# Optimization experiments

Measured on AMD Instinct MI355X. Metric: run time of the kernel, lower is better.

The kernel has to match this reference:

```python
import jax, jax.numpy as jnp
import numpy as np

N_NODES = 100000
N_EDGES = 3200000
F_IN, F_HID, F_OUT = 25, 16, 2


def gcn_conv(x, edge_index, W, b, n_nodes):
    """PyG GCNConv: out = D^-1/2 (A + I) D^-1/2 (x W) + b."""
    h = x @ W  # [N, F_out] transform first (small feature dim)
    loops = jnp.arange(n_nodes, dtype=edge_index.dtype)
    row = jnp.concatenate([edge_index[0], loops])  # sources j
    col = jnp.concatenate([edge_index[1], loops])  # targets i
    ones = jnp.ones(row.shape[0], dtype=h.dtype)
    deg = jax.ops.segment_sum(ones, col, num_segments=n_nodes)
    dinv = jnp.where(deg > 0, jax.lax.rsqrt(jnp.maximum(deg, 1.0)), 0.0)
    norm = dinv[row] * dinv[col]  # [E+N]
    msgs = h[row] * norm[:, None]  # gather + scale
    out = jax.ops.segment_sum(msgs, col, num_segments=n_nodes)
    return out + b


def setup_inputs() -> dict:
    key = jax.random.key(0)
    k1, k2, k3, k4, k5, k6 = jax.random.split(key, 6)
    x = jax.random.normal(k1, (N_NODES, F_IN), dtype=jnp.float32)
    edge_index = jax.random.randint(k2, (2, N_EDGES), 0, N_NODES, dtype=jnp.int64)
    s1 = 1.0 / np.sqrt(F_IN)
    s2 = 1.0 / np.sqrt(F_HID)
    W1 = jax.random.uniform(k3, (F_IN, F_HID), jnp.float32, -s1, s1)
    b1 = jax.random.uniform(k4, (F_HID,), jnp.float32, -s1, s1)
    W2 = jax.random.uniform(k5, (F_HID, F_OUT), jnp.float32, -s2, s2)
    b2 = jax.random.uniform(k6, (F_OUT,), jnp.float32, -s2, s2)
    return {"x": x, "edge_index": edge_index, "W1": W1, "b1": b1, "W2": W2, "b2": b2}


def reference(x, edge_index, W1, b1, W2, b2):
    n = x.shape[0]
    h = jax.nn.relu(gcn_conv(x, edge_index, W1, b1, n))
    h = gcn_conv(h, edge_index, W2, b2, n)
    return jax.nn.log_softmax(h, axis=1)
```

## Files before the change

kernel.cpp:

```cpp
#include <hip/hip_runtime.h>
#include <hip/hip_fp16.h>
#include <math.h>

#define THREADS 256
#define NPB 1024
#define SHIFT 10
#define MASK 1023
#define MAX_BINS 128
#define CAPE 36864
#define BIN_BLOCKS 512


__global__ void __launch_bounds__(256) k_bin(const int* __restrict__ row,
                                             const int* __restrict__ col,
                                             int e, int* __restrict__ binCnt,
                                             int* __restrict__ binned) {
    __shared__ int hist[MAX_BINS];
    __shared__ int cur[MAX_BINS];
    __shared__ int baseg[MAX_BINS];
    __shared__ int lofs[MAX_BINS];
    __shared__ int scn[MAX_BINS];
    extern __shared__ int dyn[];
    int per = (((e + (int)gridDim.x - 1) / (int)gridDim.x) + 3) & ~3;
    int e0 = blockIdx.x * per;
    if (e0 >= e) return;
    int e1 = min(e0 + per, e);
    int cntL = e1 - e0;
    int* sbuf  = dyn;
    int* sbuf2 = dyn + per;
    unsigned char* sbin = (unsigned char*)(dyn + 2 * per);
    int tid = threadIdx.x;
    for (int t = tid; t < MAX_BINS; t += 256) { hist[t] = 0; cur[t] = 0; }
    __syncthreads();
    int nq = cntL >> 2;
    const int4* r4 = (const int4*)(row + e0);
    const int4* c4 = (const int4*)(col + e0);
    for (int q = tid; q < nq; q += 256) {
        int4 r = r4[q], c = c4[q];
        int b0 = c.x >> SHIFT, b1 = c.y >> SHIFT, b2 = c.z >> SHIFT, b3 = c.w >> SHIFT;
        ((int4*)sbuf)[q] = make_int4((r.x << SHIFT) | (c.x & MASK),
                                     (r.y << SHIFT) | (c.y & MASK),
                                     (r.z << SHIFT) | (c.z & MASK),
                                     (r.w << SHIFT) | (c.w & MASK));
        *((uchar4*)(sbin + q * 4)) = make_uchar4((unsigned char)b0, (unsigned char)b1,
                                                 (unsigned char)b2, (unsigned char)b3);
        atomicAdd(&hist[b0], 1); atomicAdd(&hist[b1], 1);
        atomicAdd(&hist[b2], 1); atomicAdd(&hist[b3], 1);
    }
    for (int li = (nq << 2) + tid; li < cntL; li += 256) {
        int c = col[e0 + li], r = row[e0 + li], b = c >> SHIFT;
        sbuf[li] = (r << SHIFT) | (c & MASK);
        sbin[li] = (unsigned char)b;
        atomicAdd(&hist[b], 1);
    }
    __syncthreads();
    if (tid < MAX_BINS) {
        int h = hist[tid];
        baseg[tid] = (h > 0) ? atomicAdd(&binCnt[tid], h) : 0;
        scn[tid] = h;
    }
    __syncthreads();
    for (int off = 1; off < MAX_BINS; off <<= 1) {
        int a = (tid >= off && tid < MAX_BINS) ? scn[tid - off] : 0;
        __syncthreads();
        if (tid < MAX_BINS) scn[tid] += a;
        __syncthreads();
    }
    if (tid < MAX_BINS) lofs[tid] = scn[tid] - hist[tid];
    __syncthreads();
    for (int li = tid; li < cntL; li += 256) {
        int b = sbin[li];
        int p = lofs[b] + atomicAdd(&cur[b], 1);
        sbuf2[p] = sbuf[li];
    }
    __syncthreads();
    int wv = tid >> 6, ln = tid & 63;
    for (int b = wv; b < MAX_BINS; b += 4) {
        int len = hist[b];
        int lo = lofs[b];
        int gb = baseg[b];
        for (int i = ln; i < len; i += 64) {
            int pos = gb + i;
            if (pos < CAPE) binned[b * CAPE + pos] = sbuf2[lo + i];
        }
    }
}


__global__ void __launch_bounds__(1024) k_sort(const int* __restrict__ binned,
                                               const int* __restrict__ binCnt,
                                               int* __restrict__ csr,
                                               int* __restrict__ gptr,
                                               int* __restrict__ gcnt,
                                               float* __restrict__ dinv, int n) {
    __shared__ int cnt[NPB];
    __shared__ int scn[NPB];
    int b = blockIdx.x;
    int t = threadIdx.x;
    cnt[t] = 0;
    __syncthreads();
    int m = min(binCnt[b], CAPE);
    const int* eb = binned + b * CAPE;
    for (int i = t; i < m; i += 1024)
        atomicAdd(&cnt[eb[i] & MASK], 1);
    __syncthreads();
    int v = cnt[t];
    scn[t] = v;
    __syncthreads();
    for (int off = 1; off < NPB; off <<= 1) {
        int a = (t >= off) ? scn[t - off] : 0;
        __syncthreads();
        scn[t] += a;
        __syncthreads();
    }
    int excl = scn[t] - v;
    int node = b * NPB + t;
    if (node < n) {
        gptr[node] = b * CAPE + excl;
        gcnt[node] = v;
        dinv[node] = rsqrtf((float)(v + 1));
    }
    cnt[t] = excl;
    __syncthreads();
    for (int i = t; i < m; i += 1024) {
        int e = eb[i];
        int slot = atomicAdd(&cnt[e & MASK], 1);
        csr[b * CAPE + slot] = e >> SHIFT;
    }
}

__global__ void __launch_bounds__(256) k_xform1(const float* __restrict__ x,
                                                const float* __restrict__ W1,
                                                const float* __restrict__ dinv,
                                                __half* __restrict__ z1h, int n) {
    __shared__ float sW[25 * 16];
    __shared__ float tile[4][64 * 25];
    int w = threadIdx.x >> 6, lane = threadIdx.x & 63;
    for (int t = threadIdx.x; t < 25 * 16; t += 256) sW[t] = W1[t];
    long blockRow = (long)blockIdx.x * 256;
    long waveRow = blockRow + w * 64;
    const float* src = x + waveRow * 25;
    long rem = (long)n * 25 - waveRow * 25;
#pragma unroll
    for (int k = 0; k < 25; k++) {
        int idx = k * 64 + lane;
        tile[w][idx] = (idx < rem) ? src[idx] : 0.f;
    }
    __syncthreads();
    long node = blockRow + threadIdx.x;
    if (node >= n) return;
    float xi[25];
#pragma unroll
    for (int k = 0; k < 25; k++) xi[k] = tile[w][lane * 25 + k];
    float di = dinv[node];
    union { int4 v[2]; __half h[16]; } u;
#pragma unroll
    for (int c = 0; c < 16; c++) {
        float a = 0.f;
#pragma unroll
        for (int k = 0; k < 25; k++) a = fmaf(xi[k], sW[k * 16 + c], a);
        u.h[c] = __float2half(a * di);
    }
    int4* o = (int4*)(z1h + node * 16);
    o[0] = u.v[0];
    o[1] = u.v[1];
}

__global__ void k_gather1(const int* __restrict__ ptr, const int* __restrict__ cnt,
                          const int* __restrict__ csr, const __half* __restrict__ z1h,
                          const float* __restrict__ dinv,
                          const float* __restrict__ b1, const float* __restrict__ W2,
                          __half2* __restrict__ z2h, int n) {
    int g = threadIdx.x >> 3;
    int c2 = threadIdx.x & 7;
    int node = blockIdx.x * 32 + g;
    if (node >= n) return;
    const __half2* z1p = (const __half2*)z1h;
    int beg = ptr[node], d = cnt[node];
    __half2 sv = z1p[(size_t)node * 8 + c2];
    float a0 = __low2float(sv), a1 = __high2float(sv);
    int e = 0;
    for (; e + 4 <= d; e += 4) {
        int s0 = csr[beg + e], s1 = csr[beg + e + 1];
        int s2 = csr[beg + e + 2], s3 = csr[beg + e + 3];
        __half2 v0 = z1p[(size_t)s0 * 8 + c2];
        __half2 v1 = z1p[(size_t)s1 * 8 + c2];
        __half2 v2 = z1p[(size_t)s2 * 8 + c2];
        __half2 v3 = z1p[(size_t)s3 * 8 + c2];
        a0 += (__low2float(v0) + __low2float(v1)) + (__low2float(v2) + __low2float(v3));
        a1 += (__high2float(v0) + __high2float(v1)) + (__high2float(v2) + __high2float(v3));
    }
    for (; e < d; e++) {
        __half2 v = z1p[(size_t)csr[beg + e] * 8 + c2];
        a0 += __low2float(v);
        a1 += __high2float(v);
    }
    float di = dinv[node];
    int cA = c2 * 2, cB = c2 * 2 + 1;
    float hA = fmaxf(fmaf(di, a0, b1[cA]), 0.f);
    float hB = fmaxf(fmaf(di, a1, b1[cB]), 0.f);
    float p0 = hA * W2[cA * 2 + 0] + hB * W2[cB * 2 + 0];
    float p1 = hA * W2[cA * 2 + 1] + hB * W2[cB * 2 + 1];
#pragma unroll
    for (int m = 1; m < 8; m <<= 1) {
        p0 += __shfl_xor(p0, m, 8);
        p1 += __shfl_xor(p1, m, 8);
    }
    if (c2 == 0) z2h[node] = __floats2half2_rn(di * p0, di * p1);
}

__global__ void k_gather2(const int* __restrict__ ptr, const int* __restrict__ cnt,
                          const int* __restrict__ csr, const __half2* __restrict__ z2h,
                          const float* __restrict__ dinv,
                          const float* __restrict__ b2, float* __restrict__ out, int n) {
    int node = blockIdx.x * blockDim.x + threadIdx.x;
    if (node >= n) return;
    int beg = ptr[node], d = cnt[node];
    __half2 self = z2h[node];
    float a0 = __low2float(self), a1 = __high2float(self);
    int e = 0;
    for (; e + 4 <= d; e += 4) {
        __half2 v0 = z2h[csr[beg + e]];
        __half2 v1 = z2h[csr[beg + e + 1]];
        __half2 v2 = z2h[csr[beg + e + 2]];
        __half2 v3 = z2h[csr[beg + e + 3]];
        a0 += (__low2float(v0) + __low2float(v1)) + (__low2float(v2) + __low2float(v3));
        a1 += (__high2float(v0) + __high2float(v1)) + (__high2float(v2) + __high2float(v3));
    }
    for (; e < d; e++) {
        __half2 v = z2h[csr[beg + e]];
        a0 += __low2float(v);
        a1 += __high2float(v);
    }
    float di = dinv[node];
    float h0 = fmaf(di, a0, b2[0]);
    float h1 = fmaf(di, a1, b2[1]);
    float m = fmaxf(h0, h1);
    float lse = m + log1pf(expf(fminf(h0, h1) - m));
    out[(size_t)node * 2 + 0] = h0 - lse;
    out[(size_t)node * 2 + 1] = h1 - lse;
}


__global__ void k_zero(int* cnt, int n) {
    int i = blockIdx.x * blockDim.x + threadIdx.x;
    if (i < n) cnt[i] = 0;
}

__global__ void k_count_pos(const int* __restrict__ col, int e,
                            int* __restrict__ cnt, int* __restrict__ pos) {
    int i = blockIdx.x * blockDim.x + threadIdx.x;
    if (i < e) pos[i] = atomicAdd(&cnt[col[i]], 1);
}

__global__ void k_scan1(const int* __restrict__ cnt, int n,
                        int* __restrict__ excl, int* __restrict__ bsum) {
    __shared__ int s[256];
    int i = blockIdx.x * 256 + threadIdx.x;
    int v = (i < n) ? cnt[i] : 0;
    s[threadIdx.x] = v;
    __syncthreads();
    for (int off = 1; off < 256; off <<= 1) {
        int t = (threadIdx.x >= off) ? s[threadIdx.x - off] : 0;
        __syncthreads();
        s[threadIdx.x] += t;
        __syncthreads();
    }
    if (i < n) excl[i] = s[threadIdx.x] - v;
    if (threadIdx.x == 255) bsum[blockIdx.x] = s[255];
}

__global__ void k_scan2(int* __restrict__ bsum, int nb) {
    __shared__ int s[1024];
    int v = (threadIdx.x < nb) ? bsum[threadIdx.x] : 0;
    s[threadIdx.x] = v;
    __syncthreads();
    for (int off = 1; off < 1024; off <<= 1) {
        int t = (threadIdx.x >= off) ? s[threadIdx.x - off] : 0;
        __syncthreads();
        s[threadIdx.x] += t;
        __syncthreads();
    }
    if (threadIdx.x < nb) bsum[threadIdx.x] = s[threadIdx.x] - v;
}

__global__ void k_scan3(int* __restrict__ excl, const int* __restrict__ boff, int n) {
    int i = blockIdx.x * 256 + threadIdx.x;
    if (i < n) excl[i] += boff[blockIdx.x];
}

__global__ void k_place(const int* __restrict__ row, const int* __restrict__ col,
                        const int* __restrict__ pos, const int* __restrict__ ptr,
                        int e, int* __restrict__ csr) {
    int i = blockIdx.x * blockDim.x + threadIdx.x;
    if (i >= e) return;
    csr[ptr[col[i]] + pos[i]] = row[i];
}

__global__ void k_dinv_from_cnt(const int* __restrict__ cnt, float* __restrict__ dinv, int n) {
    int i = blockIdx.x * blockDim.x + threadIdx.x;
    if (i < n) dinv[i] = rsqrtf((float)(cnt[i] + 1));
}


extern "C" void kernel_launch(void* const* d_in, const int* in_sizes, int n_in,
                              void* d_out, int out_size, void* d_ws, size_t ws_size,
                              hipStream_t stream) {
    const float* x  = (const float*)d_in[0];
    const int*   ei = (const int*)d_in[1];
    const float* W1 = (const float*)d_in[2];
    const float* b1 = (const float*)d_in[3];
    const float* W2 = (const float*)d_in[4];
    const float* b2 = (const float*)d_in[5];
    float* out = (float*)d_out;

    const int N = in_sizes[0] / 25;
    const int E = in_sizes[1] / 2;
    const int* row = ei;
    const int* col = ei + E;

    const int nbins = (N + NPB - 1) / NPB;
    const int gN = (N + THREADS - 1) / THREADS;
    const int gE = (E + THREADS - 1) / THREADS;

    size_t off = 0;
    auto take = [&](size_t bytes) { size_t o = off; off = (off + bytes + 255) & ~(size_t)255; return o; };
    size_t o_binCnt = take(MAX_BINS * sizeof(int));
    size_t o_binned = take((size_t)nbins * CAPE * sizeof(int));
    size_t o_csr    = take((size_t)nbins * CAPE * sizeof(int));
    size_t o_ptr    = take((size_t)N * sizeof(int));
    size_t o_cnt    = take((size_t)N * sizeof(int));
    size_t o_dinv   = take((size_t)N * sizeof(float));
    size_t o_z1h    = take((size_t)N * 16 * sizeof(__half));
    size_t o_z2h    = take((size_t)N * sizeof(__half2));
    size_t need_v9 = off;

    double mu = (double)E / (double)nbins;
    bool cap_ok = (mu + 8.0 * sqrt(mu)) < (double)CAPE;
    const int per = (((E + BIN_BLOCKS - 1) / BIN_BLOCKS) + 3) & ~3;
    size_t dynLds = (size_t)per * 9 + 64;
    bool lds_ok = dynLds <= 60 * 1024;
    bool use_v9 = (nbins <= MAX_BINS) && (ws_size >= need_v9) &&
                  (N <= NPB * MAX_BINS) && (N < (1 << 17)) && cap_ok && lds_ok;

    char* wsb = (char*)d_ws;
    if (use_v9) {
        int*     binCnt = (int*)(wsb + o_binCnt);
        int*     binned = (int*)(wsb + o_binned);
        int*     csr    = (int*)(wsb + o_csr);
        int*     ptr    = (int*)(wsb + o_ptr);
        int*     cnt    = (int*)(wsb + o_cnt);
        float*   dinv   = (float*)(wsb + o_dinv);
        __half*  z1h    = (__half*)(wsb + o_z1h);
        __half2* z2h    = (__half2*)(wsb + o_z2h);

        hipMemsetAsync(binCnt, 0, MAX_BINS * sizeof(int), stream);
        k_bin<<<BIN_BLOCKS, 256, dynLds, stream>>>(row, col, E, binCnt, binned);
        k_sort<<<nbins, 1024, 0, stream>>>(binned, binCnt, csr, ptr, cnt, dinv, N);
        k_xform1<<<gN, 256, 0, stream>>>(x, W1, dinv, z1h, N);
        k_gather1<<<(N + 31) / 32, 256, 0, stream>>>(ptr, cnt, csr, z1h, dinv, b1, W2, z2h, N);
        k_gather2<<<gN, THREADS, 0, stream>>>(ptr, cnt, csr, z2h, dinv, b2, out, N);
    } else {
        char* w = wsb;
        int*     cnt  = (int*)w;     w += (size_t)N * sizeof(int);
        int*     ptr  = (int*)w;     w += (size_t)N * sizeof(int);
        int*     pos  = (int*)w;     w += (size_t)E * sizeof(int);
        int*     csr  = (int*)w;     w += (size_t)E * sizeof(int);
        int*     bsum = (int*)w;     w += (size_t)1024 * sizeof(int);
        float*   dinv = (float*)w;   w += (size_t)N * sizeof(float);
        __half*  z1h  = (__half*)w;  w += (size_t)N * 16 * sizeof(__half);
        __half2* z2h  = (__half2*)w; w += (size_t)N * sizeof(__half2);
        const int NB = (N + 255) / 256;

        k_zero<<<gN, THREADS, 0, stream>>>(cnt, N);
        k_count_pos<<<gE, THREADS, 0, stream>>>(col, E, cnt, pos);
        k_scan1<<<NB, 256, 0, stream>>>(cnt, N, ptr, bsum);
        k_scan2<<<1, 1024, 0, stream>>>(bsum, NB);
        k_scan3<<<NB, 256, 0, stream>>>(ptr, bsum, N);
        k_place<<<gE, THREADS, 0, stream>>>(row, col, pos, ptr, E, csr);
        k_dinv_from_cnt<<<gN, THREADS, 0, stream>>>(cnt, dinv, N);
        k_xform1<<<gN, 256, 0, stream>>>(x, W1, dinv, z1h, N);
        k_gather1<<<(N + 31) / 32, 256, 0, stream>>>(ptr, cnt, csr, z1h, dinv, b1, W2, z2h, N);
        k_gather2<<<gN, THREADS, 0, stream>>>(ptr, cnt, csr, z2h, dinv, b2, out, N);
    }
}
```

Before: 203.1 us.

## Split per-bin sort into half-bin blocks and use 8-lane groups in layer-2 gather

Measured after the change: 214.8 us. 1.06x slower.

```diff
diff --git a/kernel.cpp b/kernel.cpp
--- a/kernel.cpp
+++ b/kernel.cpp
@@ -4,10 +4,12 @@
 
 #define THREADS 256
 #define NPB 1024
+#define HNPB 512
 #define SHIFT 10
 #define MASK 1023
 #define MAX_BINS 128
 #define CAPE 36864
+#define HCAPE 18432
 #define BIN_BLOCKS 512
 
 
@@ -87,45 +89,52 @@
 }
 
 
-__global__ void __launch_bounds__(1024) k_sort(const int* __restrict__ binned,
-                                               const int* __restrict__ binCnt,
-                                               int* __restrict__ csr,
-                                               int* __restrict__ gptr,
-                                               int* __restrict__ gcnt,
-                                               float* __restrict__ dinv, int n) {
-    __shared__ int cnt[NPB];
-    __shared__ int scn[NPB];
-    int b = blockIdx.x;
+__global__ void __launch_bounds__(512) k_sort(const int* __restrict__ binned,
+                                              const int* __restrict__ binCnt,
+                                              int* __restrict__ csr,
+                                              int* __restrict__ gptr,
+                                              int* __restrict__ gcnt,
+                                              float* __restrict__ dinv, int n) {
+    __shared__ int cnt[HNPB];
+    __shared__ int scn[HNPB];
+    int b = blockIdx.x >> 1;
+    int h = blockIdx.x & 1;
     int t = threadIdx.x;
     cnt[t] = 0;
     __syncthreads();
     int m = min(binCnt[b], CAPE);
     const int* eb = binned + b * CAPE;
-    for (int i = t; i < m; i += 1024)
-        atomicAdd(&cnt[eb[i] & MASK], 1);
+    for (int i = t; i < m; i += 512) {
+        int loc = eb[i] & MASK;
+        if ((loc >> 9) == h) atomicAdd(&cnt[loc & (HNPB - 1)], 1);
+    }
     __syncthreads();
     int v = cnt[t];
     scn[t] = v;
     __syncthreads();
-    for (int off = 1; off < NPB; off <<= 1) {
+    for (int off = 1; off < HNPB; off <<= 1) {
         int a = (t >= off) ? scn[t - off] : 0;
         __syncthreads();
         scn[t] += a;
         __syncthreads();
     }
     int excl = scn[t] - v;
-    int node = b * NPB + t;
+    int node = b * NPB + h * HNPB + t;
+    int base = b * CAPE + h * HCAPE;
     if (node < n) {
-        gptr[node] = b * CAPE + excl;
+        gptr[node] = base + excl;
         gcnt[node] = v;
         dinv[node] = rsqrtf((float)(v + 1));
     }
     cnt[t] = excl;
     __syncthreads();
-    for (int i = t; i < m; i += 1024) {
+    for (int i = t; i < m; i += 512) {
         int e = eb[i];
-        int slot = atomicAdd(&cnt[e & MASK], 1);
-        csr[b * CAPE + slot] = e >> SHIFT;
+        int loc = e & MASK;
+        if ((loc >> 9) == h) {
+            int slot = atomicAdd(&cnt[loc & (HNPB - 1)], 1);
+            csr[base + slot] = e >> SHIFT;
+        }
     }
 }
 
@@ -213,32 +222,33 @@
                           const int* __restrict__ csr, const __half2* __restrict__ z2h,
                           const float* __restrict__ dinv,
                           const float* __restrict__ b2, float* __restrict__ out, int n) {
-    int node = blockIdx.x * blockDim.x + threadIdx.x;
+    int g = threadIdx.x >> 3;
+    int c = threadIdx.x & 7;
+    int node = blockIdx.x * 32 + g;
     if (node >= n) return;
     int beg = ptr[node], d = cnt[node];
-    __half2 self = z2h[node];
-    float a0 = __low2float(self), a1 = __high2float(self);
-    int e = 0;
-    for (; e + 4 <= d; e += 4) {
-        __half2 v0 = z2h[csr[beg + e]];
-        __half2 v1 = z2h[csr[beg + e + 1]];
-        __half2 v2 = z2h[csr[beg + e + 2]];
-        __half2 v3 = z2h[csr[beg + e + 3]];
-        a0 += (__low2float(v0) + __low2float(v1)) + (__low2float(v2) + __low2float(v3));
-        a1 += (__high2float(v0) + __high2float(v1)) + (__high2float(v2) + __high2float(v3));
-    }
-    for (; e < d; e++) {
+    float a0 = 0.f, a1 = 0.f;
+    for (int e = c; e < d; e += 8) {
         __half2 v = z2h[csr[beg + e]];
         a0 += __low2float(v);
         a1 += __high2float(v);
     }
-    float di = dinv[node];
-    float h0 = fmaf(di, a0, b2[0]);
-    float h1 = fmaf(di, a1, b2[1]);
-    float m = fmaxf(h0, h1);
-    float lse = m + log1pf(expf(fminf(h0, h1) - m));
-    out[(size_t)node * 2 + 0] = h0 - lse;
-    out[(size_t)node * 2 + 1] = h1 - lse;
+#pragma unroll
+    for (int m = 1; m < 8; m <<= 1) {
+        a0 += __shfl_xor(a0, m, 8);
+        a1 += __shfl_xor(a1, m, 8);
+    }
+    if (c == 0) {
+        __half2 self = z2h[node];
+        a0 += __low2float(self);
+        a1 += __high2float(self);
+        float di = dinv[node];
+        float h0 = fmaf(di, a0, b2[0]);
+        float h1 = fmaf(di, a1, b2[1]);
+        float mx = fmaxf(h0, h1);
+        float lse = mx + log1pf(expf(fminf(h0, h1) - mx));
+        ((float2*)out)[node] = make_float2(h0 - lse, h1 - lse);
+    }
 }
 
 
@@ -333,18 +343,18 @@
     size_t o_dinv   = take((size_t)N * sizeof(float));
     size_t o_z1h    = take((size_t)N * 16 * sizeof(__half));
     size_t o_z2h    = take((size_t)N * sizeof(__half2));
-    size_t need_v9 = off;
-
-    double mu = (double)E / (double)nbins;
-    bool cap_ok = (mu + 8.0 * sqrt(mu)) < (double)CAPE;
+    size_t need_v10 = off;
+
+    double mu2 = (double)E / (double)(2 * nbins);
+    bool cap_ok = (mu2 + 8.0 * sqrt(mu2)) < (double)HCAPE;
     const int per = (((E + BIN_BLOCKS - 1) / BIN_BLOCKS) + 3) & ~3;
     size_t dynLds = (size_t)per * 9 + 64;
     bool lds_ok = dynLds <= 60 * 1024;
-    bool use_v9 = (nbins <= MAX_BINS) && (ws_size >= need_v9) &&
-                  (N <= NPB * MAX_BINS) && (N < (1 << 17)) && cap_ok && lds_ok;
+    bool use_v10 = (nbins <= MAX_BINS) && (ws_size >= need_v10) &&
+                   (N <= NPB * MAX_BINS) && (N < (1 << 17)) && cap_ok && lds_ok;
 
     char* wsb = (char*)d_ws;
-    if (use_v9) {
+    if (use_v10) {
         int*     binCnt = (int*)(wsb + o_binCnt);
         int*     binned = (int*)(wsb + o_binned);
         int*     csr    = (int*)(wsb + o_csr);
@@ -356,10 +366,10 @@
 
         hipMemsetAsync(binCnt, 0, MAX_BINS * sizeof(int), stream);
         k_bin<<<BIN_BLOCKS, 256, dynLds, stream>>>(row, col, E, binCnt, binned);
-        k_sort<<<nbins, 1024, 0, stream>>>(binned, binCnt, csr, ptr, cnt, dinv, N);
+        k_sort<<<nbins * 2, 512, 0, stream>>>(binned, binCnt, csr, ptr, cnt, dinv, N);
         k_xform1<<<gN, 256, 0, stream>>>(x, W1, dinv, z1h, N);
         k_gather1<<<(N + 31) / 32, 256, 0, stream>>>(ptr, cnt, csr, z1h, dinv, b1, W2, z2h, N);
-        k_gather2<<<gN, THREADS, 0, stream>>>(ptr, cnt, csr, z2h, dinv, b2, out, N);
+        k_gather2<<<(N + 31) / 32, 256, 0, stream>>>(ptr, cnt, csr, z2h, dinv, b2, out, N);
     } else {
         char* w = wsb;
         int*     cnt  = (int*)w;     w += (size_t)N * sizeof(int);
@@ -381,6 +391,6 @@
         k_dinv_from_cnt<<<gN, THREADS, 0, stream>>>(cnt, dinv, N);
         k_xform1<<<gN, 256, 0, stream>>>(x, W1, dinv, z1h, N);
         k_gather1<<<(N + 31) / 32, 256, 0, stream>>>(ptr, cnt, csr, z1h, dinv, b1, W2, z2h, N);
-        k_gather2<<<gN, THREADS, 0, stream>>>(ptr, cnt, csr, z2h, dinv, b2, out, N);
-    }
-}
+        k_gather2<<<(N + 31) / 32, 256, 0, stream>>>(ptr, cnt, csr, z2h, dinv, b2, out, N);
+    }
+}
```
